# Optimization experiments

Hardware: AMD Instinct MI355X
Metric: run time of the kernel (lower is better)

The kernel has to match this reference:

```python
import jax, jax.numpy as jnp
import numpy as np

FILTER = [1.0, 3.0, 3.0, 1.0]
FILTER_RADIUS = len(FILTER) // 2  # = 2


def setup_inputs() -> dict:
    key = jax.random.key(0)
    x = jax.random.normal(key, (16, 128, 128, 128), dtype=jnp.float32)
    # CreateLowpassKernel(Filter, Inplace=True): outer product of the 1-D taps, normalized.
    w = np.array([FILTER], dtype=np.float32)  # [1, 4]
    k = w.T @ w                               # [4, 4]
    kernel = jnp.asarray(k / k.sum(), dtype=jnp.float32)
    return {"x": x, "kernel": kernel}


def pixel_shuffle(x, r):
    # [B, C*r*r, H, W] -> [B, C, H*r, W*r] (torch pixel_shuffle semantics)
    B, C, H, W = x.shape
    c = C // (r * r)
    x = x.reshape(B, c, r, r, H, W)
    x = x.transpose(0, 1, 4, 2, 5, 3)  # B, c, H, r, W, r
    return x.reshape(B, c, H * r, W * r)


def reference(x, kernel):
    # pixel_shuffle by 2, then upfirdn2d(up=1, down=1, padding=FilterRadius):
    # pad by FilterRadius on all sides and apply the 2-D FIR filter as a true
    # convolution (kernel flipped), depthwise across channels.
    x = pixel_shuffle(x, 2)                      # [B, C, 2H, 2W]
    B, C, H, W = x.shape
    f = jnp.flip(kernel, (0, 1))                 # true convolution -> flip taps
    w = jnp.tile(f[None, None], (C, 1, 1, 1))    # [C, 1, kh, kw] depthwise
    p = FILTER_RADIUS
    return jax.lax.conv_general_dilated(
        x, w, window_strides=(1, 1), padding=[(p, p), (p, p)],
        dimension_numbers=("NCHW", "OIHW", "NCHW"),
        feature_group_count=C)  # [B, C, 2H+1, 2W+1]
```

## Files before the change

kernel.cpp:

```cpp
#include <hip/hip_runtime.h>

constexpr int Hn = 128;
constexpr int Wn = 128;
constexpr int SH = 2 * Hn;
constexpr int OH = SH + 1;
constexpr int OW = 257;
constexpr int HW = Hn * Wn;
constexpr int TY = 65;
constexpr int NSTRIP = 4;
constexpr int NBC = 16 * 32;
constexpr int PF = 4;
constexpr int NIT = TY + 3;

__device__ __forceinline__ void barrier_lgkm_only() {
    asm volatile("s_waitcnt lgkmcnt(0)\n\ts_barrier" ::: "memory");
}

__global__ __launch_bounds__(256, 8) void upsamp_fir_lds(
    const float* __restrict__ x,
    const float* __restrict__ k4,
    float* __restrict__ out)
{
    const int tix = threadIdx.x;
    const int bc  = blockIdx.x;
    const int oh0 = blockIdx.y * TY;
    const float* xp = x + (size_t)bc * 4 * HW;

    float fh[4], fv[4];
#pragma unroll
    for (int j = 0; j < 4; ++j) fh[j] = k4[j] + k4[4+j] + k4[8+j] + k4[12+j];
#pragma unroll
    for (int i = 0; i < 4; ++i) fv[i] = k4[4*i] + k4[4*i+1] + k4[4*i+2] + k4[4*i+3];
    const float h0 = fh[3], h1 = fh[2], h2 = fh[1], h3 = fh[0];
    const float g0 = fv[3], g1 = fv[2], g2 = fv[1], g3 = fv[0];

    __shared__ float lds[2][2][132];
    if (tix < 8) {
        int b = tix >> 2, r = tix & 3;
        lds[b][r >> 1][(r & 1) ? 129 : 0] = 0.f;
    }

    const int eo       = tix < 128 ? 0 : 1;
    const int lane     = tix & 127;
    const int stageIdx = 1 + lane;

    auto xload = [&](int s) -> float {
        return xp[(size_t)(2 * (s & 1) + eo) * HW + (size_t)(s >> 1) * Wn + lane];
    };

    const int c    = tix;
    const int mi   = c >> 1;
    const int codd = c & 1;
    const bool edge = (tix == 255);

    float* const obase = out + (size_t)bc * OH * OW;

    float rr0 = 0, rr1 = 0, rr2 = 0, rr3 = 0;
    { int s = oh0 - 2; if ((unsigned)s < (unsigned)SH) rr0 = xload(s); }
    { int s = oh0 - 1; if ((unsigned)s < (unsigned)SH) rr1 = xload(s); }
    { int s = oh0;     if ((unsigned)s < (unsigned)SH) rr2 = xload(s); }
    { int s = oh0 + 1; if ((unsigned)s < (unsigned)SH) rr3 = xload(s); }

    float hm3 = 0, hm2 = 0, hm1 = 0;
    float em3 = 0, em2 = 0, em1 = 0;

    auto step = [&](int m, float& rr, int buf) {
        const int s = oh0 - 2 + m;
        lds[buf][eo][stageIdx] = rr;
        float nv = 0.f;
        const int sp = s + PF;
        if (m < NIT - PF && sp < SH) nv = xload(sp);
        rr = nv;
        barrier_lgkm_only();
        const float* EB = lds[buf][0];
        const float* OB = lds[buf][1];
        const float* P = codd ? (OB + mi) : (EB + mi);
        const float* Q = codd ? (EB + mi + 1) : (OB + mi);
        const float p0 = P[0], p1 = P[1];
        const float q0 = Q[0], q1 = Q[1];
        const float hn = h0*p0 + h1*q0 + h2*p1 + h3*q1;
        float en = 0.f;
        if (edge) {
            en = h0*EB[128] + h1*OB[128] + h2*EB[129] + h3*OB[129];
        }
        if (m >= 3) {
            const int oh = oh0 + m - 3;
            if (oh < OH) {
                float* p = obase + (size_t)oh * OW;
                p[c] = g0*hm3 + g1*hm2 + g2*hm1 + g3*hn;
                if (edge) p[256] = g0*em3 + g1*em2 + g2*em1 + g3*en;
            }
        }
        hm3 = hm2; hm2 = hm1; hm1 = hn;
        em3 = em2; em2 = em1; em1 = en;
    };

    for (int mm = 0; mm < NIT; mm += 4) {
        step(mm + 0, rr0, 0);
        step(mm + 1, rr1, 1);
        step(mm + 2, rr2, 0);
        step(mm + 3, rr3, 1);
    }
}

extern "C" void kernel_launch(void* const* d_in, const int* in_sizes, int n_in,
                              void* d_out, int out_size, void* d_ws, size_t ws_size,
                              hipStream_t stream)
{
    const float* x  = (const float*)d_in[0];
    const float* k4 = (const float*)d_in[1];
    float* out      = (float*)d_out;

    dim3 grid(NBC, NSTRIP, 1);
    upsamp_fir_lds<<<grid, dim3(256), 0, stream>>>(x, k4, out);
}
```

Before: 249.7 us.

## Process four source rows per barrier round with float2 loads and double-buffered LDS

Restructures the row-streaming loop so that each round stages four input rows into LDS at once. Each 64-thread group loads one row as float2 from both even and odd planes. This cuts barriers per output row by four and widens global loads, and the next round's loads are double-buffered against compute. It also simplifies the edge column computation, at the cost of more LDS and register use per block.

```diff
diff --git a/kernel.cpp b/kernel.cpp
--- a/kernel.cpp
+++ b/kernel.cpp
@@ -9,14 +9,13 @@
 constexpr int TY = 65;
 constexpr int NSTRIP = 4;
 constexpr int NBC = 16 * 32;
-constexpr int PF = 4;
-constexpr int NIT = TY + 3;
+constexpr int NROUND = 17;
 
 __device__ __forceinline__ void barrier_lgkm_only() {
     asm volatile("s_waitcnt lgkmcnt(0)\n\ts_barrier" ::: "memory");
 }
 
-__global__ __launch_bounds__(256, 8) void upsamp_fir_lds(
+__global__ __launch_bounds__(256, 8) void upsamp_fir_q4(
     const float* __restrict__ x,
     const float* __restrict__ k4,
     float* __restrict__ out)
@@ -31,76 +30,99 @@
     for (int j = 0; j < 4; ++j) fh[j] = k4[j] + k4[4+j] + k4[8+j] + k4[12+j];
 #pragma unroll
     for (int i = 0; i < 4; ++i) fv[i] = k4[4*i] + k4[4*i+1] + k4[4*i+2] + k4[4*i+3];
-    const float h0 = fh[3], h1 = fh[2], h2 = fh[1], h3 = fh[0];
+    const float t0 = fh[3], t1 = fh[2], t2 = fh[1], t3 = fh[0];
     const float g0 = fv[3], g1 = fv[2], g2 = fv[1], g3 = fv[0];
 
-    __shared__ float lds[2][2][132];
-    if (tix < 8) {
-        int b = tix >> 2, r = tix & 3;
-        lds[b][r >> 1][(r & 1) ? 129 : 0] = 0.f;
-    }
+    __shared__ float lds[2][4][2][132];
 
-    const int eo       = tix < 128 ? 0 : 1;
-    const int lane     = tix & 127;
-    const int stageIdx = 1 + lane;
+    const int rsel = tix >> 6;
+    const int l    = tix & 63;
 
-    auto xload = [&](int s) -> float {
-        return xp[(size_t)(2 * (s & 1) + eo) * HW + (size_t)(s >> 1) * Wn + lane];
+    auto loadRows = [&](int S, float2& e2, float2& o2) {
+        const int s = S + rsel;
+        if ((unsigned)s >= (unsigned)SH) {
+            e2 = make_float2(0.f, 0.f); o2 = e2; return;
+        }
+        const float* be = xp + (size_t)(2 * (s & 1)) * HW
+                             + (size_t)(s >> 1) * Wn + 2 * l;
+        e2 = *(const float2*)be;
+        o2 = *(const float2*)(be + HW);
+    };
+    auto stage = [&](int b, const float2& e2, const float2& o2) {
+        float* EB = &lds[b][rsel][0][0];
+        float* OB = &lds[b][rsel][1][0];
+        EB[1 + 2*l] = e2.x; EB[2 + 2*l] = e2.y;
+        OB[1 + 2*l] = o2.x; OB[2 + 2*l] = o2.y;
     };
 
     const int c    = tix;
     const int mi   = c >> 1;
     const int codd = c & 1;
     const bool edge = (tix == 255);
-
     float* const obase = out + (size_t)bc * OH * OW;
 
-    float rr0 = 0, rr1 = 0, rr2 = 0, rr3 = 0;
-    { int s = oh0 - 2; if ((unsigned)s < (unsigned)SH) rr0 = xload(s); }
-    { int s = oh0 - 1; if ((unsigned)s < (unsigned)SH) rr1 = xload(s); }
-    { int s = oh0;     if ((unsigned)s < (unsigned)SH) rr2 = xload(s); }
-    { int s = oh0 + 1; if ((unsigned)s < (unsigned)SH) rr3 = xload(s); }
+    float hp1 = 0, hp2 = 0, hp3 = 0;
+    float ep1 = 0, ep2 = 0, ep3 = 0;
 
-    float hm3 = 0, hm2 = 0, hm1 = 0;
-    float em3 = 0, em2 = 0, em1 = 0;
-
-    auto step = [&](int m, float& rr, int buf) {
-        const int s = oh0 - 2 + m;
-        lds[buf][eo][stageIdx] = rr;
-        float nv = 0.f;
-        const int sp = s + PF;
-        if (m < NIT - PF && sp < SH) nv = xload(sp);
-        rr = nv;
-        barrier_lgkm_only();
-        const float* EB = lds[buf][0];
-        const float* OB = lds[buf][1];
-        const float* P = codd ? (OB + mi) : (EB + mi);
-        const float* Q = codd ? (EB + mi + 1) : (OB + mi);
-        const float p0 = P[0], p1 = P[1];
-        const float q0 = Q[0], q1 = Q[1];
-        const float hn = h0*p0 + h1*q0 + h2*p1 + h3*q1;
-        float en = 0.f;
-        if (edge) {
-            en = h0*EB[128] + h1*OB[128] + h2*EB[129] + h3*OB[129];
+    auto computeRound = [&](int r, int b) {
+        const int S = oh0 - 2 + 4 * r;
+        float N[4], EN[4];
+#pragma unroll
+        for (int j = 0; j < 4; ++j) {
+            const float* EB = &lds[b][j][0][0];
+            const float* OB = &lds[b][j][1][0];
+            const float* P = codd ? (OB + mi)     : (EB + mi);
+            const float* Q = codd ? (EB + mi + 1) : (OB + mi);
+            const float p0 = P[0], p1 = P[1];
+            const float q0 = Q[0], q1 = Q[1];
+            N[j]  = t0*p0 + t1*q0 + t2*p1 + t3*q1;
+            EN[j] = t0*q0 + t1*p1;
         }
-        if (m >= 3) {
-            const int oh = oh0 + m - 3;
-            if (oh < OH) {
+#pragma unroll
+        for (int j = 0; j < 4; ++j) {
+            const int oh = S - 1 + j;
+            if ((r > 0 || j == 3) && oh < OH) {
+                float v, ve;
+                if (j == 0) { v = g0*hp3 + g1*hp2 + g2*hp1 + g3*N[0];
+                              ve = g0*ep3 + g1*ep2 + g2*ep1 + g3*EN[0]; }
+                if (j == 1) { v = g0*hp2 + g1*hp1 + g2*N[0] + g3*N[1];
+                              ve = g0*ep2 + g1*ep1 + g2*EN[0] + g3*EN[1]; }
+                if (j == 2) { v = g0*hp1 + g1*N[0] + g2*N[1] + g3*N[2];
+                              ve = g0*ep1 + g1*EN[0] + g2*EN[1] + g3*EN[2]; }
+                if (j == 3) { v = g0*N[0] + g1*N[1] + g2*N[2] + g3*N[3];
+                              ve = g0*EN[0] + g1*EN[1] + g2*EN[2] + g3*EN[3]; }
                 float* p = obase + (size_t)oh * OW;
-                p[c] = g0*hm3 + g1*hm2 + g2*hm1 + g3*hn;
-                if (edge) p[256] = g0*em3 + g1*em2 + g2*em1 + g3*en;
+                p[c] = v;
+                if (edge) p[256] = ve;
             }
         }
-        hm3 = hm2; hm2 = hm1; hm1 = hn;
-        em3 = em2; em2 = em1; em1 = en;
+        hp3 = N[1]; hp2 = N[2]; hp1 = N[3];
+        ep3 = EN[1]; ep2 = EN[2]; ep1 = EN[3];
     };
 
-    for (int mm = 0; mm < NIT; mm += 4) {
-        step(mm + 0, rr0, 0);
-        step(mm + 1, rr1, 1);
-        step(mm + 2, rr2, 0);
-        step(mm + 3, rr3, 1);
+    float2 eA, oA, eB, oB;
+    loadRows(oh0 - 2, eA, oA);
+    stage(0, eA, oA);
+    if (tix < 32) {
+        const int b = tix >> 4, rj = (tix >> 2) & 3, pl = (tix >> 1) & 1;
+        lds[b][rj][pl][(tix & 1) ? 129 : 0] = 0.f;
     }
+    loadRows(oh0 + 2, eB, oB);
+    __syncthreads();
+
+    for (int rr = 0; rr < NROUND - 1; rr += 2) {
+        computeRound(rr, 0);
+        stage(1, eB, oB);
+        if (rr + 2 < NROUND) loadRows(oh0 - 2 + 4*(rr + 2), eA, oA);
+        barrier_lgkm_only();
+        computeRound(rr + 1, 1);
+        if (rr + 2 < NROUND) {
+            stage(0, eA, oA);
+            if (rr + 3 < NROUND) loadRows(oh0 - 2 + 4*(rr + 3), eB, oB);
+        }
+        barrier_lgkm_only();
+    }
+    computeRound(NROUND - 1, 0);
 }
 
 extern "C" void kernel_launch(void* const* d_in, const int* in_sizes, int n_in,
@@ -112,5 +134,5 @@
     float* out      = (float*)d_out;
 
     dim3 grid(NBC, NSTRIP, 1);
-    upsamp_fir_lds<<<grid, dim3(256), 0, stream>>>(x, k4, out);
+    upsamp_fir_q4<<<grid, dim3(256), 0, stream>>>(x, k4, out);
 }
```

Result: slower. 265.1 us (+6.2%).

## Replace double-buffered staging with 4-slot LDS ring and float2 loads by two waves

Applied to the files above, without the earlier changes.

Loading is restructured so only the first two waves fetch input rows, using float2 vector loads into a four-slot LDS ring that is staged two rounds ahead and prefetched four rows ahead. The old version had all 256 threads do scalar loads into a two-buffer LDS. The edge-column horizontal tap is now computed branch-free from values already read. The aim is fewer load instructions and a deeper pipeline that hides global latency behind the per-row barrier, at the cost of more LDS and uneven load work across waves.

```diff
diff --git a/kernel.cpp b/kernel.cpp
--- a/kernel.cpp
+++ b/kernel.cpp
@@ -9,19 +9,20 @@
 constexpr int TY = 65;
 constexpr int NSTRIP = 4;
 constexpr int NBC = 16 * 32;
-constexpr int PF = 4;
 constexpr int NIT = TY + 3;
 
 __device__ __forceinline__ void barrier_lgkm_only() {
     asm volatile("s_waitcnt lgkmcnt(0)\n\ts_barrier" ::: "memory");
 }
 
-__global__ __launch_bounds__(256, 8) void upsamp_fir_lds(
+__global__ __launch_bounds__(256, 8) void upsamp_fir_ring(
     const float* __restrict__ x,
     const float* __restrict__ k4,
     float* __restrict__ out)
 {
     const int tix = threadIdx.x;
+    const int wid = tix >> 6;
+    const int l   = tix & 63;
     const int bc  = blockIdx.x;
     const int oh0 = blockIdx.y * TY;
     const float* xp = x + (size_t)bc * 4 * HW;
@@ -31,75 +32,78 @@
     for (int j = 0; j < 4; ++j) fh[j] = k4[j] + k4[4+j] + k4[8+j] + k4[12+j];
 #pragma unroll
     for (int i = 0; i < 4; ++i) fv[i] = k4[4*i] + k4[4*i+1] + k4[4*i+2] + k4[4*i+3];
-    const float h0 = fh[3], h1 = fh[2], h2 = fh[1], h3 = fh[0];
+    const float t0 = fh[3], t1 = fh[2], t2 = fh[1], t3 = fh[0];
     const float g0 = fv[3], g1 = fv[2], g2 = fv[1], g3 = fv[0];
 
-    __shared__ float lds[2][2][132];
-    if (tix < 8) {
-        int b = tix >> 2, r = tix & 3;
-        lds[b][r >> 1][(r & 1) ? 129 : 0] = 0.f;
-    }
+    __shared__ float lds[4][2][132];
 
-    const int eo       = tix < 128 ? 0 : 1;
-    const int lane     = tix & 127;
-    const int stageIdx = 1 + lane;
-
-    auto xload = [&](int s) -> float {
-        return xp[(size_t)(2 * (s & 1) + eo) * HW + (size_t)(s >> 1) * Wn + lane];
+    auto qload = [&](int s) -> float2 {
+        if ((unsigned)s >= (unsigned)SH) return make_float2(0.f, 0.f);
+        const float* b = xp + (size_t)(2 * (s & 1) + wid) * HW
+                            + (size_t)(s >> 1) * Wn + 2 * l;
+        return *(const float2*)b;
+    };
+    auto qstage = [&](int slot, float2 v) {
+        float* B = &lds[slot][wid][1 + 2 * l];
+        B[0] = v.x; B[1] = v.y;
     };
 
     const int c    = tix;
     const int mi   = c >> 1;
     const int codd = c & 1;
     const bool edge = (tix == 255);
-
     float* const obase = out + (size_t)bc * OH * OW;
 
-    float rr0 = 0, rr1 = 0, rr2 = 0, rr3 = 0;
-    { int s = oh0 - 2; if ((unsigned)s < (unsigned)SH) rr0 = xload(s); }
-    { int s = oh0 - 1; if ((unsigned)s < (unsigned)SH) rr1 = xload(s); }
-    { int s = oh0;     if ((unsigned)s < (unsigned)SH) rr2 = xload(s); }
-    { int s = oh0 + 1; if ((unsigned)s < (unsigned)SH) rr3 = xload(s); }
+    float hp1 = 0, hp2 = 0, hp3 = 0;
+    float ep1 = 0, ep2 = 0, ep3 = 0;
 
-    float hm3 = 0, hm2 = 0, hm1 = 0;
-    float em3 = 0, em2 = 0, em1 = 0;
-
-    auto step = [&](int m, float& rr, int buf) {
-        const int s = oh0 - 2 + m;
-        lds[buf][eo][stageIdx] = rr;
-        float nv = 0.f;
-        const int sp = s + PF;
-        if (m < NIT - PF && sp < SH) nv = xload(sp);
-        rr = nv;
-        barrier_lgkm_only();
-        const float* EB = lds[buf][0];
-        const float* OB = lds[buf][1];
-        const float* P = codd ? (OB + mi) : (EB + mi);
+    auto compute = [&](int r, int slot) {
+        const float* EB = &lds[slot][0][0];
+        const float* OB = &lds[slot][1][0];
+        const float* P = codd ? (OB + mi)     : (EB + mi);
         const float* Q = codd ? (EB + mi + 1) : (OB + mi);
         const float p0 = P[0], p1 = P[1];
         const float q0 = Q[0], q1 = Q[1];
-        const float hn = h0*p0 + h1*q0 + h2*p1 + h3*q1;
-        float en = 0.f;
-        if (edge) {
-            en = h0*EB[128] + h1*OB[128] + h2*EB[129] + h3*OB[129];
-        }
-        if (m >= 3) {
-            const int oh = oh0 + m - 3;
+        const float hn = t0*p0 + t1*q0 + t2*p1 + t3*q1;
+        const float en = t0*q0 + t1*p1;
+        if (r >= 3) {
+            const int oh = oh0 + r - 3;
             if (oh < OH) {
                 float* p = obase + (size_t)oh * OW;
-                p[c] = g0*hm3 + g1*hm2 + g2*hm1 + g3*hn;
-                if (edge) p[256] = g0*em3 + g1*em2 + g2*em1 + g3*en;
+                p[c] = g0*hp3 + g1*hp2 + g2*hp1 + g3*hn;
+                if (edge) p[256] = g0*ep3 + g1*ep2 + g2*ep1 + g3*en;
             }
         }
-        hm3 = hm2; hm2 = hm1; hm1 = hn;
-        em3 = em2; em2 = em1; em1 = en;
+        hp3 = hp2; hp2 = hp1; hp1 = hn;
+        ep3 = ep2; ep2 = ep1; ep1 = en;
     };
 
+    auto round = [&](int r, float2& qw, float2& ql) {
+        if (wid < 2) {
+            if (r + 2 < NIT) qstage((r + 2) & 3, qw);
+            if (r + 4 < NIT) ql = qload(oh0 - 2 + r + 4);
+        }
+        barrier_lgkm_only();
+        compute(r, r & 3);
+    };
+
+    float2 q0v = make_float2(0.f, 0.f), q1v = q0v, q2v = q0v, q3v = q0v;
+    if (wid < 2) {
+        float2 t;
+        t = qload(oh0 - 2); qstage(0, t);
+        t = qload(oh0 - 1); qstage(1, t);
+        q2v = qload(oh0);
+        q3v = qload(oh0 + 1);
+    }
+    if (tix < 16)
+        lds[tix & 3][(tix >> 2) & 1][(tix >> 3) ? 129 : 0] = 0.f;
+    __syncthreads();
+
     for (int mm = 0; mm < NIT; mm += 4) {
-        step(mm + 0, rr0, 0);
-        step(mm + 1, rr1, 1);
-        step(mm + 2, rr2, 0);
-        step(mm + 3, rr3, 1);
+        round(mm + 0, q2v, q0v);
+        round(mm + 1, q3v, q1v);
+        round(mm + 2, q0v, q2v);
+        round(mm + 3, q1v, q3v);
     }
 }
 
@@ -112,5 +116,5 @@
     float* out      = (float*)d_out;
 
     dim3 grid(NBC, NSTRIP, 1);
-    upsamp_fir_lds<<<grid, dim3(256), 0, stream>>>(x, k4, out);
+    upsamp_fir_ring<<<grid, dim3(256), 0, stream>>>(x, k4, out);
 }
```

Measured after the change: 261.7 us. +4.8%, slower.
